# Performance work log

Hardware: AMD Instinct MI355X
Metric: run time of the kernel (lower is better)

## Reference

```python
import jax, jax.numpy as jnp
import numpy as np

H = 512   # hidden_size
B = 64    # batch
P = 32    # n_prev_sents (context length)
R = 4     # n_resp
W = 64    # n_words per response


def setup_inputs() -> dict:
    key = jax.random.key(0)
    ks = jax.random.split(key, 10)
    s = 1.0 / np.sqrt(H)  # scale params to keep tanh out of hard saturation
    return {
        "context_output": jax.random.normal(ks[0], (P, B, H), jnp.float32),
        "resp_output": jax.random.normal(ks[1], (R, W, B, H), jnp.float32),
        "resp_hidden": jax.random.normal(ks[2], (R, B, H), jnp.float32),
        "W_c": jax.random.normal(ks[3], (H, H), jnp.float32) * s,
        "W_t": jax.random.normal(ks[4], (H, H), jnp.float32) * s,
        "W_a": jax.random.normal(ks[5], (H, H), jnp.float32) * s,
        "W_alpha": jax.random.normal(ks[6], (H, 1), jnp.float32) * s,
        "lin_w": jax.random.normal(ks[7], (H, H), jnp.float32) * s,    # self.linear.weight
        "lin_p_w": jax.random.normal(ks[8], (H, H), jnp.float32) * s,  # self.linear_p.weight
        "lin_x_w": jax.random.normal(ks[9], (H, H), jnp.float32) * s,  # self.linear_x.weight
    }


def reference(context_output, resp_output, resp_hidden,
              W_c, W_t, W_a, W_alpha, lin_w, lin_p_w, lin_x_w):
    # context_output: [P, B, H]; resp_output: [R, W, B, H]; resp_hidden: [R, B, H]
    R_, W_, B_, H_ = resp_output.shape
    ctx = jnp.transpose(context_output, (1, 0, 2))            # [B, P, H]
    Wctx = jnp.einsum('bph,hk->bpk', ctx, W_c)                # hoisted: constant over words
    w_alpha = W_alpha[:, 0]                                   # [H]

    def step(resp_atten, resp_t):
        # resp_atten, resp_t: [R, B, H]
        w = resp_t @ W_t + resp_atten @ W_a                   # [R, B, H]
        M = jnp.tanh(Wctx[None] + w[:, :, None, :])           # [R, B, P, H]
        alpha = jax.nn.softmax(jnp.einsum('rbph,h->rbp', M, w_alpha), axis=-1)  # [R, B, P]
        atten_t = jnp.einsum('rbp,bph->rbh', alpha, ctx)      # [R, B, H]
        new_atten = atten_t + jnp.tanh(resp_atten @ lin_w.T)  # recurrence
        return new_atten, alpha

    init = jnp.zeros((R_, B_, H_), resp_output.dtype)
    resp_atten, alphas = jax.lax.scan(step, init, jnp.swapaxes(resp_output, 0, 1))  # scan over words

    resp_c = jnp.tanh(resp_atten @ lin_p_w.T + resp_hidden @ lin_x_w.T)  # [R, B, H]
    alpha_vec = jnp.swapaxes(alphas, 0, 1)                               # [R, W, B, P]
    return resp_c, alpha_vec
```

## Files before the change

kernel.cpp:

```cpp
#include <hip/hip_runtime.h>
#include <math.h>

#define Hd 512
#define Bd 64
#define Pd 32
#define Rd 4
#define Wd 64

typedef _Float16 h2v __attribute__((ext_vector_type(2)));

__device__ __forceinline__ float tanh_fast(float x) {
    float e = __expf(x + x);
    return 1.f - __fdividef(2.f, 1.f + e);
}

__device__ __forceinline__ float d2(unsigned a, unsigned b, float c) {
    return __builtin_amdgcn_fdot2(__builtin_bit_cast(h2v, a),
                                  __builtin_bit_cast(h2v, b), c, false);
}

__global__ void k_prep_wa(const float* __restrict__ Wa, const float* __restrict__ lin_w,
                          float* __restrict__ WAc) {
    __shared__ float tile[32][33];
    int bx = blockIdx.x, by = blockIdx.y;
    int lane = threadIdx.x & 31, ty = threadIdx.x >> 5;
    for (int k = 0; k < 32; k += 8) {
        int y = by * 32 + ty + k;
        WAc[(size_t)y * 1024 + bx * 32 + lane] = Wa[(size_t)y * Hd + bx * 32 + lane];
    }
    int x = bx * 32 + lane;
    for (int k = 0; k < 32; k += 8) {
        int y = by * 32 + ty + k;
        tile[ty + k][lane] = lin_w[(size_t)y * Hd + x];
    }
    __syncthreads();
    int xo = by * 32 + lane;
    for (int k = 0; k < 32; k += 8) {
        int yo = bx * 32 + ty + k;
        WAc[(size_t)yo * 1024 + 512 + xo] = tile[lane][ty + k];
    }
}

__global__ __launch_bounds__(256) void k_pack(const float* __restrict__ WAc,
                                              unsigned* __restrict__ WAp) {
    int idx = blockIdx.x * 256 + threadIdx.x;
    int h2 = idx >> 10, c = idx & 1023;
    h2v p;
    p.x = (_Float16)WAc[((size_t)(2 * h2)) * 1024 + c];
    p.y = (_Float16)WAc[((size_t)(2 * h2 + 1)) * 1024 + c];
    WAp[idx] = __builtin_bit_cast(unsigned, p);
}

__global__ void k_wctx(const float* __restrict__ ctx_pbh, const float* __restrict__ Wc,
                       float* __restrict__ Wctx) {
    __shared__ float As[16][Hd];
    int r0 = blockIdx.x * 16;
    int tid = threadIdx.x;
    for (int rr = 0; rr < 16; ++rr) {
        int bp = r0 + rr;
        int b = bp >> 5, p = bp & 31;
        const float* src = ctx_pbh + ((size_t)p * Bd + b) * Hd;
        for (int h = tid; h < Hd; h += 256) As[rr][h] = src[h];
    }
    __syncthreads();
    int c0 = tid, c1 = tid + 256;
    float acc0[16], acc1[16];
    #pragma unroll
    for (int rr = 0; rr < 16; ++rr) { acc0[rr] = 0.f; acc1[rr] = 0.f; }
    for (int h = 0; h < Hd; ++h) {
        float w0 = Wc[(size_t)h * Hd + c0], w1 = Wc[(size_t)h * Hd + c1];
        #pragma unroll
        for (int rr = 0; rr < 16; ++rr) {
            float a = As[rr][h];
            acc0[rr] += a * w0;
            acc1[rr] += a * w1;
        }
    }
    for (int rr = 0; rr < 16; ++rr) {
        Wctx[(size_t)(r0 + rr) * Hd + c0] = acc0[rr];
        Wctx[(size_t)(r0 + rr) * Hd + c1] = acc1[rr];
    }
}

__global__ __launch_bounds__(256) void k_rw(const float* __restrict__ resp,
                                            const float* __restrict__ Wt,
                                            unsigned short* __restrict__ rwh) {
    __shared__ float As[16][Hd];
    int gr0 = blockIdx.x * 16;
    int tid = threadIdx.x;
    for (int rr = 0; rr < 16; ++rr) {
        int gr = gr0 + rr;
        int t = gr >> 8, row = gr & 255;
        int r = row >> 6, bb = row & 63;
        const float* src = resp + (((size_t)(r * Wd + t)) * Bd + bb) * Hd;
        for (int h = tid; h < Hd; h += 256) As[rr][h] = src[h];
    }
    __syncthreads();
    int c0 = tid, c1 = tid + 256;
    float acc0[16], acc1[16];
    #pragma unroll
    for (int rr = 0; rr < 16; ++rr) { acc0[rr] = 0.f; acc1[rr] = 0.f; }
    for (int h = 0; h < Hd; ++h) {
        float w0 = Wt[(size_t)h * Hd + c0], w1 = Wt[(size_t)h * Hd + c1];
        #pragma unroll
        for (int rr = 0; rr < 16; ++rr) {
            float a = As[rr][h];
            acc0[rr] += a * w0;
            acc1[rr] += a * w1;
        }
    }
    for (int rr = 0; rr < 16; ++rr) {
        rwh[(size_t)(gr0 + rr) * Hd + c0] =
            __builtin_bit_cast(unsigned short, (_Float16)acc0[rr]);
        rwh[(size_t)(gr0 + rr) * Hd + c1] =
            __builtin_bit_cast(unsigned short, (_Float16)acc1[rr]);
    }
}

__global__ __launch_bounds__(1024, 4) void k_scan(
    const float* __restrict__ ctx,
    const unsigned short* __restrict__ rwh,
    const unsigned* __restrict__ WAp,
    const float* __restrict__ Wctx,
    const float* __restrict__ walpha,
    const float* __restrict__ hidden,
    const float* __restrict__ lin_p,
    const float* __restrict__ lin_x,
    float* __restrict__ out_resp,
    float* __restrict__ out_alpha)
{
    extern __shared__ float dynS[];
    float* sCtx   = dynS;
    float* sWctx  = dynS + 16384;
    float* sPart  = dynS + 32768;
    float* sW     = dynS + 36864;
    float* sAtten = dynS + 37888;
    unsigned* sAttenH = (unsigned*)(dynS + 38400);
    __shared__ float sWal[Hd];
    __shared__ float scS[Pd];

    const int bid = blockIdx.x;
    const int r_ = bid >> 6, b_ = bid & 63;
    const int tid = threadIdx.x;

    for (int i = tid; i < 4096; i += 1024) {
        int p = i >> 7, h4 = (i & 127) << 2;
        *(float4*)&sCtx[(p << 9) + h4] =
            *(const float4*)&ctx[((size_t)(p * Bd + b_)) * Hd + h4];
        *(float4*)&sWctx[(p << 9) + h4] =
            *(const float4*)&Wctx[((size_t)(b_ * Pd + p)) * Hd + h4];
    }
    if (tid < Hd) sWal[tid] = walpha[tid];
    if (tid < 256) sAttenH[tid] = 0u;
    __syncthreads();

    const int qid = tid >> 8;
    const int cq  = (tid & 255) << 2;
    const unsigned* __restrict__ wap = WAp + ((size_t)(qid << 6) << 10) + cq;
    const unsigned* __restrict__ ah  = sAttenH + (qid << 6);

    const int pB = tid >> 5, hcB = tid & 31;

    for (int t = 0; t < Wd; ++t) {
        float rwf = 0.f;
        if (tid < Hd) {
            unsigned short u = rwh[((size_t)(t * 256 + bid) << 9) + tid];
            rwf = (float)__builtin_bit_cast(_Float16, u);
        }

        if (t > 0) {
            float4 acc = make_float4(0.f, 0.f, 0.f, 0.f);
            #pragma unroll 4
            for (int jq = 0; jq < 16; ++jq) {
                const unsigned* wq = wap + ((size_t)jq << 12);
                uint4 w0 = *(const uint4*)(wq);
                uint4 w1 = *(const uint4*)(wq + 1024);
                uint4 w2 = *(const uint4*)(wq + 2048);
                uint4 w3 = *(const uint4*)(wq + 3072);
                uint4 a4 = *(const uint4*)(ah + (jq << 2));
                acc.x = d2(a4.x, w0.x, acc.x); acc.y = d2(a4.x, w0.y, acc.y);
                acc.z = d2(a4.x, w0.z, acc.z); acc.w = d2(a4.x, w0.w, acc.w);
                acc.x = d2(a4.y, w1.x, acc.x); acc.y = d2(a4.y, w1.y, acc.y);
                acc.z = d2(a4.y, w1.z, acc.z); acc.w = d2(a4.y, w1.w, acc.w);
                acc.x = d2(a4.z, w2.x, acc.x); acc.y = d2(a4.z, w2.y, acc.y);
                acc.z = d2(a4.z, w2.z, acc.z); acc.w = d2(a4.z, w2.w, acc.w);
                acc.x = d2(a4.w, w3.x, acc.x); acc.y = d2(a4.w, w3.y, acc.y);
                acc.z = d2(a4.w, w3.z, acc.z); acc.w = d2(a4.w, w3.w, acc.w);
            }
            *(float4*)&sPart[(qid << 10) + cq] = acc;
            __syncthreads();
        }

        {
            float s = rwf;
            if (t > 0)
                s += sPart[tid] + sPart[1024 + tid] + sPart[2048 + tid] + sPart[3072 + tid];
            sW[tid] = s;
        }
        __syncthreads();

        {
            const float* __restrict__ wrow = sWctx + (pB << 9);
            float sc = 0.f;
            #pragma unroll
            for (int k = 0; k < 4; ++k) {
                int h4 = (k << 7) + (hcB << 2);
                float4 wc  = *(const float4*)&wrow[h4];
                float4 wal = *(const float4*)&sWal[h4];
                float4 v   = *(const float4*)&sW[h4];
                sc += tanh_fast(wc.x+v.x)*wal.x + tanh_fast(wc.y+v.y)*wal.y
                    + tanh_fast(wc.z+v.z)*wal.z + tanh_fast(wc.w+v.w)*wal.w;
            }
            #pragma unroll
            for (int off = 16; off; off >>= 1) sc += __shfl_down(sc, off, 32);
            if (hcB == 0) scS[pB] = sc;
        }
        __syncthreads();

        if (tid < Hd) {
            float sv[Pd];
            #pragma unroll
            for (int p = 0; p < Pd; ++p) sv[p] = scS[p];
            float m = sv[0];
            #pragma unroll
            for (int p = 1; p < Pd; ++p) m = fmaxf(m, sv[p]);
            float sum = 0.f;
            #pragma unroll
            for (int p = 0; p < Pd; ++p) { sv[p] = __expf(sv[p] - m); sum += sv[p]; }
            float inv = __fdividef(1.f, sum);
            if (tid < Pd)
                out_alpha[(((size_t)r_ * Wd + t) * Bd + b_) * Pd + tid] = sv[tid] * inv;
            float a = 0.f;
            #pragma unroll 8
            for (int p = 0; p < Pd; ++p) a += sv[p] * sCtx[(p << 9) + tid];
            a = a * inv + tanh_fast(sW[Hd + tid]);
            sAtten[tid] = a;
            float an = __shfl_down(a, 1, 64);
            if (!(tid & 1)) {
                h2v ph; ph.x = (_Float16)a; ph.y = (_Float16)an;
                sAttenH[tid >> 1] = __builtin_bit_cast(unsigned, ph);
            }
        }
        __syncthreads();
    }

    if (tid < Hd) sPart[tid] = hidden[((size_t)(r_ * Bd + b_)) * Hd + tid];
    __syncthreads();
    {
        const int half = tid >> 9;
        const int c = tid & 511;
        const int hb = half << 8;
        const float* __restrict__ lp = lin_p + (size_t)c * Hd + hb;
        const float* __restrict__ lx = lin_x + (size_t)c * Hd + hb;
        float f = 0.f;
        #pragma unroll 2
        for (int h = 0; h < 256; h += 4) {
            float4 lpv = *(const float4*)(lp + h);
            float4 lxv = *(const float4*)(lx + h);
            float4 aa  = *(const float4*)&sAtten[hb + h];
            float4 hh  = *(const float4*)&sPart[hb + h];
            f += aa.x*lpv.x + aa.y*lpv.y + aa.z*lpv.z + aa.w*lpv.w
               + hh.x*lxv.x + hh.y*lxv.y + hh.z*lxv.z + hh.w*lxv.w;
        }
        sPart[1024 + (half << 9) + c] = f;
    }
    __syncthreads();
    if (tid < Hd) {
        float f = sPart[1024 + tid] + sPart[1536 + tid];
        out_resp[((size_t)(r_ * Bd + b_)) * Hd + tid] = tanh_fast(f);
    }
}

extern "C" void kernel_launch(void* const* d_in, const int* in_sizes, int n_in,
                              void* d_out, int out_size, void* d_ws, size_t ws_size,
                              hipStream_t stream) {
    const float* ctx    = (const float*)d_in[0];
    const float* resp   = (const float*)d_in[1];
    const float* hidden = (const float*)d_in[2];
    const float* Wc     = (const float*)d_in[3];
    const float* Wt     = (const float*)d_in[4];
    const float* Wa     = (const float*)d_in[5];
    const float* Walpha = (const float*)d_in[6];
    const float* lin_w  = (const float*)d_in[7];
    const float* lin_p  = (const float*)d_in[8];
    const float* lin_x  = (const float*)d_in[9];

    float* out = (float*)d_out;
    float* resp_c_out = out;
    float* alpha_out  = out + Rd * Bd * Hd;

    float* ws   = (float*)d_ws;
    float* WAc  = ws;
    float* Wctx = ws + 524288;
    unsigned short* rwh = (unsigned short*)(ws + 1572864);
    unsigned* WAp = (unsigned*)(ws + 5767168);

    dim3 g16(16, 16);
    k_prep_wa<<<g16, 256, 0, stream>>>(Wa, lin_w, WAc);
    k_pack<<<1024, 256, 0, stream>>>(WAc, WAp);
    k_wctx<<<128, 256, 0, stream>>>(ctx, Wc, Wctx);
    k_rw<<<1024, 256, 0, stream>>>(resp, Wt, rwh);

    const int dyn_lds = 154624;
    static bool s_attr = false;
    if (!s_attr) {
        hipFuncSetAttribute((const void*)k_scan,
                            hipFuncAttributeMaxDynamicSharedMemorySize, dyn_lds);
        s_attr = true;
    }
    k_scan<<<256, 1024, dyn_lds, stream>>>(ctx, rwh, WAp, Wctx, Walpha, hidden,
                                           lin_p, lin_x, resp_c_out, alpha_out);
}
```

Baseline: 1.114 ms.

## Split recurrent matvec across 4 blocks per batch with global-memory barriers

The scan kernel now partitions the per-step W_a/lin_w matvec by output column across the 4 blocks that share a batch element. Each block computes a quarter of the columns for all 4 responses, exchanges partial results and fp16 attention vectors through global memory, and synchronizes with per-batch atomic counters under a cooperative launch. This cuts the weight bytes each block streams per step by four, at the cost of two spin barriers per step. Preprocessing also changes: W_a and W_t packing is fused into one kernel, and the response projection uses fp16 dot2 with larger tiles.

```diff
diff --git a/kernel.cpp b/kernel.cpp
--- a/kernel.cpp
+++ b/kernel.cpp
@@ -19,44 +19,45 @@
                                   __builtin_bit_cast(h2v, b), c, false);
 }
 
-__global__ void k_prep_wa(const float* __restrict__ Wa, const float* __restrict__ lin_w,
-                          float* __restrict__ WAc) {
-    __shared__ float tile[32][33];
+__device__ __forceinline__ unsigned pk(float a, float b) {
+    h2v p; p.x = (_Float16)a; p.y = (_Float16)b;
+    return __builtin_bit_cast(unsigned, p);
+}
+
+__global__ __launch_bounds__(256) void k_prep(const float* __restrict__ Wa,
+                                              const float* __restrict__ lin_w,
+                                              const float* __restrict__ Wt,
+                                              unsigned* __restrict__ WAp,
+                                              unsigned* __restrict__ Wtp) {
+    __shared__ unsigned tile[32][33];
     int bx = blockIdx.x, by = blockIdx.y;
     int lane = threadIdx.x & 31, ty = threadIdx.x >> 5;
     for (int k = 0; k < 32; k += 8) {
-        int y = by * 32 + ty + k;
-        WAc[(size_t)y * 1024 + bx * 32 + lane] = Wa[(size_t)y * Hd + bx * 32 + lane];
-    }
-    int x = bx * 32 + lane;
+        int h2 = by * 32 + ty + k, c = bx * 32 + lane;
+        WAp[(size_t)h2 * 1024 + c] = pk(Wa[(size_t)(2 * h2) * Hd + c],
+                                        Wa[(size_t)(2 * h2 + 1) * Hd + c]);
+        Wtp[(size_t)h2 * 512 + c]  = pk(Wt[(size_t)(2 * h2) * Hd + c],
+                                        Wt[(size_t)(2 * h2 + 1) * Hd + c]);
+    }
     for (int k = 0; k < 32; k += 8) {
-        int y = by * 32 + ty + k;
-        tile[ty + k][lane] = lin_w[(size_t)y * Hd + x];
-    }
-    __syncthreads();
-    int xo = by * 32 + lane;
+        int c_src = bx * 32 + ty + k, h2 = by * 32 + lane;
+        float2 v = *(const float2*)&lin_w[(size_t)c_src * Hd + 2 * h2];
+        tile[ty + k][lane] = pk(v.x, v.y);
+    }
+    __syncthreads();
     for (int k = 0; k < 32; k += 8) {
-        int yo = bx * 32 + ty + k;
-        WAc[(size_t)yo * 1024 + 512 + xo] = tile[lane][ty + k];
-    }
-}
-
-__global__ __launch_bounds__(256) void k_pack(const float* __restrict__ WAc,
-                                              unsigned* __restrict__ WAp) {
-    int idx = blockIdx.x * 256 + threadIdx.x;
-    int h2 = idx >> 10, c = idx & 1023;
-    h2v p;
-    p.x = (_Float16)WAc[((size_t)(2 * h2)) * 1024 + c];
-    p.y = (_Float16)WAc[((size_t)(2 * h2 + 1)) * 1024 + c];
-    WAp[idx] = __builtin_bit_cast(unsigned, p);
-}
-
-__global__ void k_wctx(const float* __restrict__ ctx_pbh, const float* __restrict__ Wc,
-                       float* __restrict__ Wctx) {
-    __shared__ float As[16][Hd];
-    int r0 = blockIdx.x * 16;
+        int h2o = by * 32 + ty + k, co = bx * 32 + lane;
+        WAp[(size_t)h2o * 1024 + 512 + co] = tile[lane][ty + k];
+    }
+}
+
+__global__ __launch_bounds__(256) void k_wctx(const float* __restrict__ ctx_pbh,
+                                              const float* __restrict__ Wc,
+                                              float* __restrict__ Wctx) {
+    __shared__ float As[32][Hd];
+    int r0 = blockIdx.x * 32;
     int tid = threadIdx.x;
-    for (int rr = 0; rr < 16; ++rr) {
+    for (int rr = 0; rr < 32; ++rr) {
         int bp = r0 + rr;
         int b = bp >> 5, p = bp & 31;
         const float* src = ctx_pbh + ((size_t)p * Bd + b) * Hd;
@@ -64,57 +65,59 @@
     }
     __syncthreads();
     int c0 = tid, c1 = tid + 256;
-    float acc0[16], acc1[16];
+    float acc0[32], acc1[32];
     #pragma unroll
-    for (int rr = 0; rr < 16; ++rr) { acc0[rr] = 0.f; acc1[rr] = 0.f; }
+    for (int rr = 0; rr < 32; ++rr) { acc0[rr] = 0.f; acc1[rr] = 0.f; }
     for (int h = 0; h < Hd; ++h) {
         float w0 = Wc[(size_t)h * Hd + c0], w1 = Wc[(size_t)h * Hd + c1];
         #pragma unroll
-        for (int rr = 0; rr < 16; ++rr) {
+        for (int rr = 0; rr < 32; ++rr) {
             float a = As[rr][h];
             acc0[rr] += a * w0;
             acc1[rr] += a * w1;
         }
     }
-    for (int rr = 0; rr < 16; ++rr) {
+    for (int rr = 0; rr < 32; ++rr) {
         Wctx[(size_t)(r0 + rr) * Hd + c0] = acc0[rr];
         Wctx[(size_t)(r0 + rr) * Hd + c1] = acc1[rr];
     }
 }
 
-__global__ __launch_bounds__(256) void k_rw(const float* __restrict__ resp,
-                                            const float* __restrict__ Wt,
+__global__ __launch_bounds__(512) void k_rw(const float* __restrict__ resp,
+                                            const unsigned* __restrict__ Wtp,
                                             unsigned short* __restrict__ rwh) {
-    __shared__ float As[16][Hd];
-    int gr0 = blockIdx.x * 16;
-    int tid = threadIdx.x;
-    for (int rr = 0; rr < 16; ++rr) {
+    __shared__ unsigned As[32 * 256];
+    int gr0 = blockIdx.x * 32, tid = threadIdx.x;
+    for (int i = tid; i < 32 * 256; i += 512) {
+        int rr = i >> 8, h2 = i & 255;
         int gr = gr0 + rr;
-        int t = gr >> 8, row = gr & 255;
-        int r = row >> 6, bb = row & 63;
-        const float* src = resp + (((size_t)(r * Wd + t)) * Bd + bb) * Hd;
-        for (int h = tid; h < Hd; h += 256) As[rr][h] = src[h];
-    }
-    __syncthreads();
-    int c0 = tid, c1 = tid + 256;
-    float acc0[16], acc1[16];
+        int t = gr >> 8, row = gr & 255, r = row >> 6, bb = row & 63;
+        float2 v = *(const float2*)(resp + (((size_t)(r * Wd + t)) * Bd + bb) * Hd + (h2 << 1));
+        As[i] = pk(v.x, v.y);
+    }
+    __syncthreads();
+    float acc[32];
     #pragma unroll
-    for (int rr = 0; rr < 16; ++rr) { acc0[rr] = 0.f; acc1[rr] = 0.f; }
-    for (int h = 0; h < Hd; ++h) {
-        float w0 = Wt[(size_t)h * Hd + c0], w1 = Wt[(size_t)h * Hd + c1];
+    for (int rr = 0; rr < 32; ++rr) acc[rr] = 0.f;
+    const int c = tid;
+    #pragma unroll 1
+    for (int h2 = 0; h2 < 256; h2 += 4) {
+        unsigned w0 = Wtp[((h2 + 0) << 9) + c];
+        unsigned w1 = Wtp[((h2 + 1) << 9) + c];
+        unsigned w2 = Wtp[((h2 + 2) << 9) + c];
+        unsigned w3 = Wtp[((h2 + 3) << 9) + c];
         #pragma unroll
-        for (int rr = 0; rr < 16; ++rr) {
-            float a = As[rr][h];
-            acc0[rr] += a * w0;
-            acc1[rr] += a * w1;
-        }
-    }
-    for (int rr = 0; rr < 16; ++rr) {
-        rwh[(size_t)(gr0 + rr) * Hd + c0] =
-            __builtin_bit_cast(unsigned short, (_Float16)acc0[rr]);
-        rwh[(size_t)(gr0 + rr) * Hd + c1] =
-            __builtin_bit_cast(unsigned short, (_Float16)acc1[rr]);
-    }
+        for (int rr = 0; rr < 32; ++rr) {
+            uint4 a4 = *(const uint4*)&As[(rr << 8) + h2];
+            float s = acc[rr];
+            s = d2(a4.x, w0, s); s = d2(a4.y, w1, s);
+            s = d2(a4.z, w2, s); s = d2(a4.w, w3, s);
+            acc[rr] = s;
+        }
+    }
+    for (int rr = 0; rr < 32; ++rr)
+        rwh[((size_t)(gr0 + rr) << 9) + c] =
+            __builtin_bit_cast(unsigned short, (_Float16)acc[rr]);
 }
 
 __global__ __launch_bounds__(1024, 4) void k_scan(
@@ -127,7 +130,11 @@
     const float* __restrict__ lin_p,
     const float* __restrict__ lin_x,
     float* __restrict__ out_resp,
-    float* __restrict__ out_alpha)
+    float* __restrict__ out_alpha,
+    float* __restrict__ w_glob,
+    unsigned* __restrict__ atten_glob,
+    unsigned* __restrict__ cnt_a,
+    unsigned* __restrict__ cnt_b)
 {
     extern __shared__ float dynS[];
     float* sCtx   = dynS;
@@ -140,7 +147,7 @@
     __shared__ float scS[Pd];
 
     const int bid = blockIdx.x;
-    const int r_ = bid >> 6, b_ = bid & 63;
+    const int b_ = bid >> 2, j_ = bid & 3;
     const int tid = threadIdx.x;
 
     for (int i = tid; i < 4096; i += 1024) {
@@ -151,25 +158,34 @@
             *(const float4*)&Wctx[((size_t)(b_ * Pd + p)) * Hd + h4];
     }
     if (tid < Hd) sWal[tid] = walpha[tid];
-    if (tid < 256) sAttenH[tid] = 0u;
+    if (tid < 256) sAttenH[(j_ << 8) + tid] = 0u;
     __syncthreads();
 
     const int qid = tid >> 8;
-    const int cq  = (tid & 255) << 2;
-    const unsigned* __restrict__ wap = WAp + ((size_t)(qid << 6) << 10) + cq;
-    const unsigned* __restrict__ ah  = sAttenH + (qid << 6);
-
+    const int rr  = (tid >> 6) & 3;
+    const int c4  = (tid & 63) << 2;
+    const unsigned* __restrict__ wap =
+        WAp + ((size_t)(qid << 6) << 10) + (j_ << 8) + c4;
     const int pB = tid >> 5, hcB = tid & 31;
 
-    for (int t = 0; t < Wd; ++t) {
+    unsigned tgt = 4u;
+    for (int t = 0; t < Wd; ++t, tgt += 4u) {
         float rwf = 0.f;
         if (tid < Hd) {
-            unsigned short u = rwh[((size_t)(t * 256 + bid) << 9) + tid];
+            unsigned short u = rwh[(((size_t)t * 256 + (j_ << 6) + b_) << 9) + tid];
             rwf = (float)__builtin_bit_cast(_Float16, u);
         }
 
         if (t > 0) {
+            if (tid < 768) {
+                int rx = tid >> 8; rx += (rx >= j_) ? 1 : 0;
+                sAttenH[(rx << 8) + (tid & 255)] =
+                    atten_glob[(((b_ << 2) + rx) << 8) + (tid & 255)];
+            }
+            __syncthreads();
+
             float4 acc = make_float4(0.f, 0.f, 0.f, 0.f);
+            const unsigned* __restrict__ ah = sAttenH + (rr << 8) + (qid << 6);
             #pragma unroll 4
             for (int jq = 0; jq < 16; ++jq) {
                 const unsigned* wq = wap + ((size_t)jq << 12);
@@ -187,15 +203,33 @@
                 acc.x = d2(a4.w, w3.x, acc.x); acc.y = d2(a4.w, w3.y, acc.y);
                 acc.z = d2(a4.w, w3.z, acc.z); acc.w = d2(a4.w, w3.w, acc.w);
             }
-            *(float4*)&sPart[(qid << 10) + cq] = acc;
+            *(float4*)&sPart[(((qid << 2) + rr) << 8) + c4] = acc;
             __syncthreads();
-        }
-
-        {
-            float s = rwf;
-            if (t > 0)
-                s += sPart[tid] + sPart[1024 + tid] + sPart[2048 + tid] + sPart[3072 + tid];
-            sW[tid] = s;
+
+            {
+                int r = tid >> 8, c = tid & 255;
+                float s = sPart[((0 + r) << 8) + c] + sPart[((4 + r) << 8) + c]
+                        + sPart[((8 + r) << 8) + c] + sPart[((12 + r) << 8) + c];
+                w_glob[(((size_t)(b_ << 2) + r) << 10) + (j_ << 8) + c] = s;
+            }
+        }
+
+        __syncthreads();
+        if (tid == 0) {
+            __threadfence();
+            __hip_atomic_fetch_add(&cnt_a[b_], 1u, __ATOMIC_RELEASE, __HIP_MEMORY_SCOPE_AGENT);
+            while (__hip_atomic_load(&cnt_a[b_], __ATOMIC_ACQUIRE, __HIP_MEMORY_SCOPE_AGENT) < tgt)
+                __builtin_amdgcn_s_sleep(2);
+            __threadfence();
+        }
+        __syncthreads();
+
+        if (t > 0) {
+            float v = w_glob[(((size_t)(b_ << 2) + j_) << 10) + tid];
+            if (tid < Hd) v += rwf;
+            sW[tid] = v;
+        } else {
+            sW[tid] = (tid < Hd) ? rwf : 0.f;
         }
         __syncthreads();
 
@@ -229,7 +263,7 @@
             for (int p = 0; p < Pd; ++p) { sv[p] = __expf(sv[p] - m); sum += sv[p]; }
             float inv = __fdividef(1.f, sum);
             if (tid < Pd)
-                out_alpha[(((size_t)r_ * Wd + t) * Bd + b_) * Pd + tid] = sv[tid] * inv;
+                out_alpha[(((size_t)j_ * Wd + t) * Bd + b_) * Pd + tid] = sv[tid] * inv;
             float a = 0.f;
             #pragma unroll 8
             for (int p = 0; p < Pd; ++p) a += sv[p] * sCtx[(p << 9) + tid];
@@ -237,14 +271,24 @@
             sAtten[tid] = a;
             float an = __shfl_down(a, 1, 64);
             if (!(tid & 1)) {
-                h2v ph; ph.x = (_Float16)a; ph.y = (_Float16)an;
-                sAttenH[tid >> 1] = __builtin_bit_cast(unsigned, ph);
-            }
-        }
-        __syncthreads();
-    }
-
-    if (tid < Hd) sPart[tid] = hidden[((size_t)(r_ * Bd + b_)) * Hd + tid];
+                unsigned ph = pk(a, an);
+                sAttenH[(j_ << 8) + (tid >> 1)] = ph;
+                atten_glob[(((b_ << 2) + j_) << 8) + (tid >> 1)] = ph;
+            }
+        }
+
+        __syncthreads();
+        if (tid == 0) {
+            __threadfence();
+            __hip_atomic_fetch_add(&cnt_b[b_], 1u, __ATOMIC_RELEASE, __HIP_MEMORY_SCOPE_AGENT);
+            while (__hip_atomic_load(&cnt_b[b_], __ATOMIC_ACQUIRE, __HIP_MEMORY_SCOPE_AGENT) < tgt)
+                __builtin_amdgcn_s_sleep(2);
+            __threadfence();
+        }
+        __syncthreads();
+    }
+
+    if (tid < Hd) sPart[tid] = hidden[((size_t)(j_ * Bd + b_)) * Hd + tid];
     __syncthreads();
     {
         const int half = tid >> 9;
@@ -267,7 +311,7 @@
     __syncthreads();
     if (tid < Hd) {
         float f = sPart[1024 + tid] + sPart[1536 + tid];
-        out_resp[((size_t)(r_ * Bd + b_)) * Hd + tid] = tanh_fast(f);
+        out_resp[((size_t)(j_ * Bd + b_)) * Hd + tid] = tanh_fast(f);
     }
 }
 
@@ -289,25 +333,34 @@
     float* resp_c_out = out;
     float* alpha_out  = out + Rd * Bd * Hd;
 
-    float* ws   = (float*)d_ws;
-    float* WAc  = ws;
-    float* Wctx = ws + 524288;
-    unsigned short* rwh = (unsigned short*)(ws + 1572864);
-    unsigned* WAp = (unsigned*)(ws + 5767168);
-
-    dim3 g16(16, 16);
-    k_prep_wa<<<g16, 256, 0, stream>>>(Wa, lin_w, WAc);
-    k_pack<<<1024, 256, 0, stream>>>(WAc, WAp);
-    k_wctx<<<128, 256, 0, stream>>>(ctx, Wc, Wctx);
-    k_rw<<<1024, 256, 0, stream>>>(resp, Wt, rwh);
-
-    const int dyn_lds = 154624;
+    float* ws = (float*)d_ws;
+    unsigned* WAp = (unsigned*)ws;
+    unsigned* Wtp = (unsigned*)(ws + 262144);
+    float* Wctx   = ws + 393216;
+    unsigned short* rwh = (unsigned short*)(ws + 1441792);
+    float* w_glob = ws + 5636096;
+    unsigned* atten_glob = (unsigned*)(ws + 5898240);
+    unsigned* cnt_a = (unsigned*)(ws + 5963776);
+    unsigned* cnt_b = cnt_a + 64;
+
+    k_prep<<<dim3(16, 8), 256, 0, stream>>>(Wa, lin_w, Wt, WAp, Wtp);
+    k_wctx<<<64, 256, 0, stream>>>(ctx, Wc, Wctx);
+    k_rw<<<512, 512, 0, stream>>>(resp, Wtp, rwh);
+    hipMemsetAsync(cnt_a, 0, 128 * sizeof(unsigned), stream);
+
+    const int dyn_lds = 157696;
     static bool s_attr = false;
     if (!s_attr) {
         hipFuncSetAttribute((const void*)k_scan,
                             hipFuncAttributeMaxDynamicSharedMemorySize, dyn_lds);
         s_attr = true;
     }
-    k_scan<<<256, 1024, dyn_lds, stream>>>(ctx, rwh, WAp, Wctx, Walpha, hidden,
-                                           lin_p, lin_x, resp_c_out, alpha_out);
-}
+    void* args[] = {
+        (void*)&ctx, (void*)&rwh, (void*)&WAp, (void*)&Wctx, (void*)&Walpha,
+        (void*)&hidden, (void*)&lin_p, (void*)&lin_x,
+        (void*)&resp_c_out, (void*)&alpha_out,
+        (void*)&w_glob, (void*)&atten_glob, (void*)&cnt_a, (void*)&cnt_b
+    };
+    hipLaunchCooperativeKernel((const void*)k_scan, dim3(256), dim3(1024),
+                               args, dyn_lds, stream);
+}
```

Result: slower. 3.362 ms (+201.7%).
